# Kernel optimization log

Hardware: AMD Instinct MI355X
Metric: run time of the kernel (lower is better)

The kernel has to match this reference:

```python
import jax, jax.numpy as jnp
import numpy as np

B, T, C, W, H, HID = 64, 1024, 256, 28, 28, 512


def setup_inputs() -> dict:
    key = jax.random.key(0)
    k1, k2, k3, k4, k5, k6 = jax.random.split(key, 6)
    text = jax.random.normal(k1, (B, T), dtype=jnp.float32)
    vision = jax.random.normal(k2, (B, C, W, H), dtype=jnp.float32)
    s1 = 1.0 / np.sqrt(T + C)
    s2 = 1.0 / np.sqrt(HID)
    W1 = jax.random.uniform(k3, (T + C, HID), jnp.float32, -s1, s1)
    b1 = jax.random.uniform(k4, (HID,), jnp.float32, -s1, s1)
    W2 = jax.random.uniform(k5, (HID, 1), jnp.float32, -s2, s2)
    b2 = jax.random.uniform(k6, (1,), jnp.float32, -s2, s2)
    return {"text": text, "vision": vision, "W1": W1, "b1": b1, "W2": W2, "b2": b2}


def reference(text, vision, W1, b1, W2, b2):
    b, c, w, h = vision.shape
    p = w * h
    # pixels in (i*height + j) order, matching the torch double loop / view
    pixels = vision.transpose(0, 2, 3, 1).reshape(b, p, c)  # (B, P, C)
    text_b = jnp.broadcast_to(text[:, None, :], (b, p, text.shape[1]))
    feat = jnp.concatenate([text_b, pixels], axis=-1)        # (B, P, T+C)
    hidden = jax.nn.relu(jnp.einsum("bpf,fh->bph", feat, W1) + b1)
    scores = (jnp.einsum("bph,ho->bpo", hidden, W2) + b2)[..., 0]  # (B, P)
    weights = jax.nn.softmax(scores, axis=1)                 # (B, P)
    pooled = jnp.einsum("bpc,bp->bc", pixels, weights)       # (B, C)
    return jnp.concatenate([pooled, text], axis=1)           # (B, C+T)
```

## Files before the change

kernel.cpp:

```cpp
#include <hip/hip_runtime.h>

#define BB  64
#define TT  1024
#define CC  256
#define PP  784
#define HID 512
#define FF  1280

typedef float v4f __attribute__((ext_vector_type(4)));
typedef short v8s __attribute__((ext_vector_type(8)));

__device__ inline unsigned int bf16_rne_bits(float x) {
    unsigned int u = __float_as_uint(x);
    unsigned int r = u + 0x7FFFu + ((u >> 16) & 1u);
    return r & 0xFFFF0000u;
}

__device__ inline void barrier_lds_only() {
    asm volatile("s_waitcnt lgkmcnt(0)" ::: "memory");
    __builtin_amdgcn_s_barrier();
}

__global__ __launch_bounds__(256) void k_w1t(const float* __restrict__ W1,
                                             unsigned short* __restrict__ w1t_hi,
                                             unsigned short* __restrict__ w1t_lo) {
    const int id = blockIdx.x * 256 + threadIdx.x;
    const int ks = id >> 11;
    const int h  = (id >> 2) & 511;
    const int g  = id & 3;
    const float* W1v = W1 + (size_t)TT * HID;
    unsigned int hw[4], lw[4];
    #pragma unroll
    for (int k = 0; k < 4; ++k) {
        const int c0 = ks * 32 + g * 8 + 2 * k;
        float x0 = W1v[(size_t)c0 * HID + h];
        float x1 = W1v[(size_t)(c0 + 1) * HID + h];
        unsigned int h0 = bf16_rne_bits(x0), h1 = bf16_rne_bits(x1);
        unsigned int l0 = bf16_rne_bits(x0 - __uint_as_float(h0));
        unsigned int l1 = bf16_rne_bits(x1 - __uint_as_float(h1));
        hw[k] = (h0 >> 16) | (h1 & 0xFFFF0000u);
        lw[k] = (l0 >> 16) | (l1 & 0xFFFF0000u);
    }
    *(int4*)(&w1t_hi[(size_t)id * 8]) = make_int4(hw[0], hw[1], hw[2], hw[3]);
    *(int4*)(&w1t_lo[(size_t)id * 8]) = make_int4(lw[0], lw[1], lw[2], lw[3]);
}

__global__ __launch_bounds__(512) void k_text_gemm(const float* __restrict__ text,
                                                   const float* __restrict__ W1,
                                                   float* __restrict__ tbp) {
    const int b  = blockIdx.x;
    const int ks = blockIdx.y;
    const int t  = threadIdx.x;
    __shared__ float st[128];
    if (t < 128) st[t] = text[b * TT + ks * 128 + t];
    __syncthreads();
    float acc = 0.f;
    const float* wp = W1 + (size_t)(ks * 128) * HID + t;
    #pragma unroll 4
    for (int k = 0; k < 128; ++k)
        acc = fmaf(st[k], wp[(size_t)k * HID], acc);
    tbp[(b * 8 + ks) * HID + t] = acc;
}

__global__ __launch_bounds__(1024, 4) void k_vision_mfma(
        const float* __restrict__ vision,
        const unsigned short* __restrict__ w1t_hi,
        const unsigned short* __restrict__ w1t_lo,
        const float* __restrict__ b1,
        const float* __restrict__ W2,
        const float* __restrict__ tbp,
        float* __restrict__ scores) {
    const int ptile = blockIdx.x;
    const int b     = blockIdx.y;
    const int tid   = threadIdx.x;
    const int lane  = tid & 63;
    const int w     = tid >> 6;
    const int l15   = lane & 15, lg = lane >> 4;

    __shared__ char albuf[2][14336];
    __shared__ float sred[16 * 112];

    v4f acc[7][2];
    #pragma unroll
    for (int m = 0; m < 7; ++m) {
        acc[m][0] = (v4f){0.f, 0.f, 0.f, 0.f};
        acc[m][1] = (v4f){0.f, 0.f, 0.f, 0.f};
    }

    const size_t vbase = (size_t)b * (CC * PP) + ptile * 112;
    const int spx = tid >> 3;
    const int scg = tid & 7;
    const bool stg = (tid < 896);

    float xa[4], xb[4];

    #define A_LOAD(XV, KS) do { \
        _Pragma("unroll") for (int j = 0; j < 4; ++j) { \
            const int c_ = (KS) * 32 + scg * 4 + j; \
            XV[j] = vision[vbase + (size_t)c_ * PP + spx]; } } while (0)

    #define A_WRITE(BUF, XV) do { \
        unsigned int h0_ = bf16_rne_bits(XV[0]); \
        unsigned int h1_ = bf16_rne_bits(XV[1]); \
        unsigned int h2_ = bf16_rne_bits(XV[2]); \
        unsigned int h3_ = bf16_rne_bits(XV[3]); \
        unsigned int l0_ = bf16_rne_bits(XV[0] - __uint_as_float(h0_)); \
        unsigned int l1_ = bf16_rne_bits(XV[1] - __uint_as_float(h1_)); \
        unsigned int l2_ = bf16_rne_bits(XV[2] - __uint_as_float(h2_)); \
        unsigned int l3_ = bf16_rne_bits(XV[3] - __uint_as_float(h3_)); \
        int2 hp_ = make_int2((h0_ >> 16) | (h1_ & 0xFFFF0000u), \
                             (h2_ >> 16) | (h3_ & 0xFFFF0000u)); \
        int2 lp_ = make_int2((l0_ >> 16) | (l1_ & 0xFFFF0000u), \
                             (l2_ >> 16) | (l3_ & 0xFFFF0000u)); \
        *(int2*)(&albuf[BUF][spx * 64 + scg * 8])        = hp_; \
        *(int2*)(&albuf[BUF][7168 + spx * 64 + scg * 8]) = lp_; } while (0)

    const int bfr = ((w * 32 + l15) * 4 + lg) * 8;

    #define COMPUTE(KS, BUF) do { \
        const unsigned short* bph_ = w1t_hi + (size_t)(KS) * 16384 + bfr; \
        const unsigned short* bpl_ = w1t_lo + (size_t)(KS) * 16384 + bfr; \
        const v8s bh0 = *(const v8s*)(bph_); \
        const v8s bh1 = *(const v8s*)(bph_ + 512); \
        const v8s bl0 = *(const v8s*)(bpl_); \
        const v8s bl1 = *(const v8s*)(bpl_ + 512); \
        const char* ab_ = &albuf[BUF][0]; \
        v8s ahr[7]; \
        _Pragma("unroll") for (int m = 0; m < 7; ++m) \
            ahr[m] = *(const v8s*)(ab_ + (m * 16 + l15) * 64 + lg * 16); \
        _Pragma("unroll") for (int m = 0; m < 7; ++m) \
            acc[m][0] = __builtin_amdgcn_mfma_f32_16x16x32_bf16(ahr[m], bh0, acc[m][0], 0, 0, 0); \
        _Pragma("unroll") for (int m = 0; m < 7; ++m) \
            acc[m][1] = __builtin_amdgcn_mfma_f32_16x16x32_bf16(ahr[m], bh1, acc[m][1], 0, 0, 0); \
        _Pragma("unroll") for (int m = 0; m < 7; ++m) \
            acc[m][0] = __builtin_amdgcn_mfma_f32_16x16x32_bf16(ahr[m], bl0, acc[m][0], 0, 0, 0); \
        _Pragma("unroll") for (int m = 0; m < 7; ++m) \
            acc[m][1] = __builtin_amdgcn_mfma_f32_16x16x32_bf16(ahr[m], bl1, acc[m][1], 0, 0, 0); \
        _Pragma("unroll") for (int m = 0; m < 7; ++m) { \
            const v8s alr = *(const v8s*)(ab_ + 7168 + (m * 16 + l15) * 64 + lg * 16); \
            acc[m][0] = __builtin_amdgcn_mfma_f32_16x16x32_bf16(alr, bh0, acc[m][0], 0, 0, 0); \
            acc[m][1] = __builtin_amdgcn_mfma_f32_16x16x32_bf16(alr, bh1, acc[m][1], 0, 0, 0); \
        } } while (0)

    if (stg) { A_LOAD(xa, 0); A_LOAD(xb, 1); A_WRITE(0, xa); }
    barrier_lds_only();

    for (int s = 0; s < 8; s += 2) {
        if (stg && s + 2 < 8) A_LOAD(xa, s + 2);
        COMPUTE(s, 0);
        if (stg) A_WRITE(1, xb);
        barrier_lds_only();
        if (stg && s + 3 < 8) A_LOAD(xb, s + 3);
        COMPUTE(s + 1, 1);
        if (stg && s + 2 < 8) A_WRITE(0, xa);
        barrier_lds_only();
    }

    float tbn[2], w2n[2];
    #pragma unroll
    for (int nn = 0; nn < 2; ++nn) {
        const int h = w * 32 + nn * 16 + l15;
        const float* tp = tbp + (size_t)b * 8 * HID + h;
        float tv = b1[h];
        #pragma unroll
        for (int q = 0; q < 8; ++q) tv += tp[q * HID];
        tbn[nn] = tv;
        w2n[nn] = W2[h];
    }
    #pragma unroll
    for (int m = 0; m < 7; ++m) {
        #pragma unroll
        for (int r = 0; r < 4; ++r) {
            float s = 0.f;
            #pragma unroll
            for (int nn = 0; nn < 2; ++nn)
                s += fmaxf(acc[m][nn][r] + tbn[nn], 0.f) * w2n[nn];
            s += __shfl_xor(s, 1, 64);
            s += __shfl_xor(s, 2, 64);
            s += __shfl_xor(s, 4, 64);
            s += __shfl_xor(s, 8, 64);
            if (l15 == 0) sred[w * 112 + m * 16 + lg * 4 + r] = s;
        }
    }
    __syncthreads();
    if (tid < 112) {
        float s = 0.f;
        #pragma unroll
        for (int q = 0; q < 16; ++q) s += sred[q * 112 + tid];
        scores[b * PP + ptile * 112 + tid] = s;
    }
    #undef A_LOAD
    #undef A_WRITE
    #undef COMPUTE
}

__global__ __launch_bounds__(256) void k_softmax_copy(float* __restrict__ sw,
                                                      const float* __restrict__ text,
                                                      float* __restrict__ out) {
    const int b   = blockIdx.x;
    const int tid = threadIdx.x;
    const int lane = tid & 63, wid = tid >> 6;
    __shared__ float red[4];

    float v[4]; int cnt = 0;
    float m = -3.4e38f;
    for (int p = tid; p < PP; p += 256) { v[cnt] = sw[b * PP + p]; m = fmaxf(m, v[cnt]); ++cnt; }
    #pragma unroll
    for (int off = 32; off > 0; off >>= 1) m = fmaxf(m, __shfl_xor(m, off, 64));
    if (lane == 0) red[wid] = m;
    __syncthreads();
    m = fmaxf(fmaxf(red[0], red[1]), fmaxf(red[2], red[3]));
    __syncthreads();

    float ssum = 0.f;
    for (int i = 0; i < cnt; ++i) { v[i] = expf(v[i] - m); ssum += v[i]; }
    #pragma unroll
    for (int off = 32; off > 0; off >>= 1) ssum += __shfl_xor(ssum, off, 64);
    if (lane == 0) red[wid] = ssum;
    __syncthreads();
    const float inv = 1.f / (red[0] + red[1] + red[2] + red[3]);

    cnt = 0;
    for (int p = tid; p < PP; p += 256) sw[b * PP + p] = v[cnt++] * inv;

    for (int j = tid; j < TT; j += 256) out[b * FF + CC + j] = text[b * TT + j];
}

__global__ __launch_bounds__(256) void k_pool(const float* __restrict__ vision,
                                              const float* __restrict__ wts,
                                              float* __restrict__ out) {
    const int cg = blockIdx.x;
    const int b  = blockIdx.y;
    const int tid = threadIdx.x, lane = tid & 63, wid = tid >> 6;
    __shared__ float wl[PP];
    {
        const int i = tid * 4;
        if (i < PP) *(float4*)&wl[i] = *(const float4*)&wts[b * PP + i];
    }
    __syncthreads();
    #pragma unroll
    for (int ci = 0; ci < 8; ++ci) {
        const int c = cg * 32 + wid * 8 + ci;
        const float* vr = vision + (size_t)b * (CC * PP) + (size_t)c * PP;
        float acc = 0.f;
        #pragma unroll
        for (int k = 0; k < 4; ++k) {
            const int p4 = (lane + 64 * k) * 4;
            if (p4 < PP) {
                const float4 vv = *(const float4*)(vr + p4);
                const float4 ww = *(const float4*)&wl[p4];
                acc = fmaf(vv.x, ww.x, acc);
                acc = fmaf(vv.y, ww.y, acc);
                acc = fmaf(vv.z, ww.z, acc);
                acc = fmaf(vv.w, ww.w, acc);
            }
        }
        #pragma unroll
        for (int off = 32; off > 0; off >>= 1) acc += __shfl_xor(acc, off, 64);
        if (lane == 0) out[b * FF + c] = acc;
    }
}

extern "C" void kernel_launch(void* const* d_in, const int* in_sizes, int n_in,
                              void* d_out, int out_size, void* d_ws, size_t ws_size,
                              hipStream_t stream) {
    const float* text   = (const float*)d_in[0];
    const float* vision = (const float*)d_in[1];
    const float* W1     = (const float*)d_in[2];
    const float* b1     = (const float*)d_in[3];
    const float* W2     = (const float*)d_in[4];
    float* out = (float*)d_out;

    float* tbp = (float*)d_ws;
    float* sw  = tbp + BB * 8 * HID;
    unsigned short* w1t_hi = (unsigned short*)(sw + BB * PP);
    unsigned short* w1t_lo = w1t_hi + 131072;

    k_w1t        <<<64, 256, 0, stream>>>(W1, w1t_hi, w1t_lo);
    k_text_gemm  <<<dim3(BB, 8), 512, 0, stream>>>(text, W1, tbp);
    k_vision_mfma<<<dim3(7, BB), 1024, 0, stream>>>(vision, w1t_hi, w1t_lo,
                                                    b1, W2, tbp, sw);
    k_softmax_copy<<<BB, 256, 0, stream>>>(sw, text, out);
    k_pool       <<<dim3(8, BB), 256, 0, stream>>>(vision, sw, out);
}
```

Baseline: 191.7 us.

## Split vision MFMA kernel across hidden quarters with 256-thread blocks

The vision GEMM kernel now launches 4x more blocks of 256 threads, each handling a quarter of the hidden dimension for a 112-pixel tile. Each block writes partial scores to a four-slice buffer, and the softmax kernel sums the four slices. Staging uses 16 channels per thread with wider LDS stores. The goal is more, smaller blocks for better occupancy and scheduling. The cost is that each vision tile is loaded and bf16-split four times, once per hidden quarter, adding global traffic and conversion work.

```diff
diff --git a/kernel.cpp b/kernel.cpp
--- a/kernel.cpp
+++ b/kernel.cpp
@@ -62,23 +62,24 @@
     tbp[(b * 8 + ks) * HID + t] = acc;
 }
 
-__global__ __launch_bounds__(1024, 4) void k_vision_mfma(
+__global__ __launch_bounds__(256, 3) void k_vision_mfma(
         const float* __restrict__ vision,
         const unsigned short* __restrict__ w1t_hi,
         const unsigned short* __restrict__ w1t_lo,
         const float* __restrict__ b1,
         const float* __restrict__ W2,
         const float* __restrict__ tbp,
-        float* __restrict__ scores) {
+        float* __restrict__ spart) {
     const int ptile = blockIdx.x;
-    const int b     = blockIdx.y;
+    const int hh    = blockIdx.y;
+    const int b     = blockIdx.z;
     const int tid   = threadIdx.x;
     const int lane  = tid & 63;
     const int w     = tid >> 6;
     const int l15   = lane & 15, lg = lane >> 4;
 
     __shared__ char albuf[2][14336];
-    __shared__ float sred[16 * 112];
+    __shared__ float sred[4 * 112];
 
     v4f acc[7][2];
     #pragma unroll
@@ -88,34 +89,33 @@
     }
 
     const size_t vbase = (size_t)b * (CC * PP) + ptile * 112;
-    const int spx = tid >> 3;
-    const int scg = tid & 7;
-    const bool stg = (tid < 896);
-
-    float xa[4], xb[4];
+    const int spx = tid >> 1, sch = tid & 1;
+    const bool stg = (tid < 224);
+
+    float xa[16], xb[16];
 
     #define A_LOAD(XV, KS) do { \
-        _Pragma("unroll") for (int j = 0; j < 4; ++j) { \
-            const int c_ = (KS) * 32 + scg * 4 + j; \
+        _Pragma("unroll") for (int j = 0; j < 16; ++j) { \
+            const int c_ = (KS) * 32 + sch * 16 + j; \
             XV[j] = vision[vbase + (size_t)c_ * PP + spx]; } } while (0)
 
     #define A_WRITE(BUF, XV) do { \
-        unsigned int h0_ = bf16_rne_bits(XV[0]); \
-        unsigned int h1_ = bf16_rne_bits(XV[1]); \
-        unsigned int h2_ = bf16_rne_bits(XV[2]); \
-        unsigned int h3_ = bf16_rne_bits(XV[3]); \
-        unsigned int l0_ = bf16_rne_bits(XV[0] - __uint_as_float(h0_)); \
-        unsigned int l1_ = bf16_rne_bits(XV[1] - __uint_as_float(h1_)); \
-        unsigned int l2_ = bf16_rne_bits(XV[2] - __uint_as_float(h2_)); \
-        unsigned int l3_ = bf16_rne_bits(XV[3] - __uint_as_float(h3_)); \
-        int2 hp_ = make_int2((h0_ >> 16) | (h1_ & 0xFFFF0000u), \
-                             (h2_ >> 16) | (h3_ & 0xFFFF0000u)); \
-        int2 lp_ = make_int2((l0_ >> 16) | (l1_ & 0xFFFF0000u), \
-                             (l2_ >> 16) | (l3_ & 0xFFFF0000u)); \
-        *(int2*)(&albuf[BUF][spx * 64 + scg * 8])        = hp_; \
-        *(int2*)(&albuf[BUF][7168 + spx * 64 + scg * 8]) = lp_; } while (0)
-
-    const int bfr = ((w * 32 + l15) * 4 + lg) * 8;
+        unsigned int hw[8], lw[8]; \
+        _Pragma("unroll") for (int q = 0; q < 8; ++q) { \
+            unsigned int h0 = bf16_rne_bits(XV[2 * q]); \
+            unsigned int h1 = bf16_rne_bits(XV[2 * q + 1]); \
+            unsigned int l0 = bf16_rne_bits(XV[2 * q] - __uint_as_float(h0)); \
+            unsigned int l1 = bf16_rne_bits(XV[2 * q + 1] - __uint_as_float(h1)); \
+            hw[q] = (h0 >> 16) | (h1 & 0xFFFF0000u); \
+            lw[q] = (l0 >> 16) | (l1 & 0xFFFF0000u); } \
+        int4* ah = (int4*)(&albuf[BUF][0]) + (spx * 4 + sch * 2); \
+        int4* al = (int4*)(&albuf[BUF][7168]) + (spx * 4 + sch * 2); \
+        ah[0] = make_int4(hw[0], hw[1], hw[2], hw[3]); \
+        ah[1] = make_int4(hw[4], hw[5], hw[6], hw[7]); \
+        al[0] = make_int4(lw[0], lw[1], lw[2], lw[3]); \
+        al[1] = make_int4(lw[4], lw[5], lw[6], lw[7]); } while (0)
+
+    const int bfr = (hh * 128 + w * 32 + l15) * 32 + lg * 8;
 
     #define COMPUTE(KS, BUF) do { \
         const unsigned short* bph_ = w1t_hi + (size_t)(KS) * 16384 + bfr; \
@@ -159,7 +159,7 @@
     float tbn[2], w2n[2];
     #pragma unroll
     for (int nn = 0; nn < 2; ++nn) {
-        const int h = w * 32 + nn * 16 + l15;
+        const int h = hh * 128 + w * 32 + nn * 16 + l15;
         const float* tp = tbp + (size_t)b * 8 * HID + h;
         float tv = b1[h];
         #pragma unroll
@@ -184,10 +184,8 @@
     }
     __syncthreads();
     if (tid < 112) {
-        float s = 0.f;
-        #pragma unroll
-        for (int q = 0; q < 16; ++q) s += sred[q * 112 + tid];
-        scores[b * PP + ptile * 112 + tid] = s;
+        float s = sred[tid] + sred[112 + tid] + sred[224 + tid] + sred[336 + tid];
+        spart[((size_t)hh * BB + b) * PP + ptile * 112 + tid] = s;
     }
     #undef A_LOAD
     #undef A_WRITE
@@ -201,10 +199,15 @@
     const int tid = threadIdx.x;
     const int lane = tid & 63, wid = tid >> 6;
     __shared__ float red[4];
+    const size_t pl = (size_t)BB * PP;
 
     float v[4]; int cnt = 0;
     float m = -3.4e38f;
-    for (int p = tid; p < PP; p += 256) { v[cnt] = sw[b * PP + p]; m = fmaxf(m, v[cnt]); ++cnt; }
+    for (int p = tid; p < PP; p += 256) {
+        const size_t o = (size_t)b * PP + p;
+        v[cnt] = sw[o] + sw[pl + o] + sw[2 * pl + o] + sw[3 * pl + o];
+        m = fmaxf(m, v[cnt]); ++cnt;
+    }
     #pragma unroll
     for (int off = 32; off > 0; off >>= 1) m = fmaxf(m, __shfl_xor(m, off, 64));
     if (lane == 0) red[wid] = m;
@@ -221,7 +224,7 @@
     const float inv = 1.f / (red[0] + red[1] + red[2] + red[3]);
 
     cnt = 0;
-    for (int p = tid; p < PP; p += 256) sw[b * PP + p] = v[cnt++] * inv;
+    for (int p = tid; p < PP; p += 256) sw[(size_t)b * PP + p] = v[cnt++] * inv;
 
     for (int j = tid; j < TT; j += 256) out[b * FF + CC + j] = text[b * TT + j];
 }
@@ -235,7 +238,7 @@
     __shared__ float wl[PP];
     {
         const int i = tid * 4;
-        if (i < PP) *(float4*)&wl[i] = *(const float4*)&wts[b * PP + i];
+        if (i < PP) *(float4*)&wl[i] = *(const float4*)&wts[(size_t)b * PP + i];
     }
     __syncthreads();
     #pragma unroll
@@ -273,13 +276,13 @@
 
     float* tbp = (float*)d_ws;
     float* sw  = tbp + BB * 8 * HID;
-    unsigned short* w1t_hi = (unsigned short*)(sw + BB * PP);
+    unsigned short* w1t_hi = (unsigned short*)(sw + 4 * BB * PP);
     unsigned short* w1t_lo = w1t_hi + 131072;
 
     k_w1t        <<<64, 256, 0, stream>>>(W1, w1t_hi, w1t_lo);
     k_text_gemm  <<<dim3(BB, 8), 512, 0, stream>>>(text, W1, tbp);
-    k_vision_mfma<<<dim3(7, BB), 1024, 0, stream>>>(vision, w1t_hi, w1t_lo,
-                                                    b1, W2, tbp, sw);
+    k_vision_mfma<<<dim3(7, 4, BB), 256, 0, stream>>>(vision, w1t_hi, w1t_lo,
+                                                      b1, W2, tbp, sw);
     k_softmax_copy<<<BB, 256, 0, stream>>>(sw, text, out);
     k_pool       <<<dim3(8, BB), 256, 0, stream>>>(vision, sw, out);
 }
```

Result: faster. 178.3 us (-7.0%).
